# Kernel optimization log

Measured on AMD Instinct MI355X. Metric: run time of the kernel, lower is better.

## Reference

```python
import jax, jax.numpy as jnp
import numpy as np

EPS = 1e-6

def layer_norm(x, g, b):
    m = jnp.mean(x, axis=-1, keepdims=True)
    v = jnp.mean(jnp.square(x - m), axis=-1, keepdims=True)
    return (x - m) * jax.lax.rsqrt(v + EPS) * g + b

def setup_inputs() -> dict:
    key = jax.random.key(0)
    ks = jax.random.split(key, 12)
    B, L, D, Dff, SK = 8, 4096, 512, 2048, 128
    s = 0.02
    return {
        "x": jax.random.normal(ks[0], (B, L, D), jnp.float32),
        "Wq": jax.random.normal(ks[1], (D, D), jnp.float32) * s,
        "bq": jnp.zeros((D,), jnp.float32),
        "Wk": jax.random.normal(ks[2], (D, D), jnp.float32) * s,
        "bk": jnp.zeros((D,), jnp.float32),
        "Wv": jax.random.normal(ks[3], (D, D), jnp.float32) * s,
        "bv": jnp.zeros((D,), jnp.float32),
        "Wo": jax.random.normal(ks[4], (D, D), jnp.float32) * s,
        "bo": jnp.zeros((D,), jnp.float32),
        "g1": jnp.ones((D,), jnp.float32),
        "b1": jnp.zeros((D,), jnp.float32),
        "W1f": jax.random.normal(ks[5], (D, Dff), jnp.float32) * s,
        "b1f": jnp.zeros((Dff,), jnp.float32),
        "W2f": jax.random.normal(ks[6], (Dff, D), jnp.float32) * s,
        "b2f": jnp.zeros((D,), jnp.float32),
        "g2": jnp.ones((D,), jnp.float32),
        "b2": jnp.zeros((D,), jnp.float32),
        "sample_idx": jax.random.randint(ks[7], (SK,), 0, L, jnp.int64),
    }

NUM_HEADS = 8
TOP_U = 128

def prob_sparse_attention(x, Wq, bq, Wk, bk, Wv, bv, Wo, bo, sample_idx):
    B, L, D = x.shape
    H = NUM_HEADS
    dh = D // H
    scale = 1.0 / jnp.sqrt(jnp.asarray(dh, x.dtype))
    # projections -> [B, H, L, dh]
    def split_heads(t):
        return t.reshape(B, L, H, dh).transpose(0, 2, 1, 3)
    Q = split_heads(x @ Wq + bq)
    K = split_heads(x @ Wk + bk)
    V = split_heads(x @ Wv + bv)
    # sparsity measurement on a sampled key subset: [B, H, L, SK]
    K_samp = K[:, :, sample_idx, :]
    s_samp = jnp.einsum('bhld,bhsd->bhls', Q, K_samp)
    M = jnp.max(s_samp, axis=-1) - jnp.mean(s_samp, axis=-1)  # [B, H, L]
    _, top_idx = jax.lax.top_k(M, TOP_U)  # [B, H, u]
    # gather top-u queries: [B, H, u, dh]
    Q_top = jnp.take_along_axis(Q, top_idx[..., None], axis=2)
    scores = jnp.einsum('bhud,bhld->bhul', Q_top, K) * scale  # [B, H, u, L]
    attn = jax.nn.softmax(scores, axis=-1)
    ctx_top = jnp.einsum('bhul,bhld->bhud', attn, V)  # [B, H, u, dh]
    # lazy queries get mean(V)
    meanV = jnp.mean(V, axis=2, keepdims=True)  # [B, H, 1, dh]
    ctx = jnp.broadcast_to(meanV, (B, H, L, dh))
    bi = jnp.arange(B)[:, None, None]
    hi = jnp.arange(H)[None, :, None]
    ctx = ctx.at[bi, hi, top_idx].set(ctx_top)
    out = ctx.transpose(0, 2, 1, 3).reshape(B, L, D)
    return out @ Wo + bo

def reference(x, Wq, bq, Wk, bk, Wv, bv, Wo, bo, g1, b1, W1f, b1f, W2f, b2f, g2, b2, sample_idx):
    attn_out = prob_sparse_attention(x, Wq, bq, Wk, bk, Wv, bv, Wo, bo, sample_idx)
    x1 = layer_norm(x + attn_out, g1, b1)
    ffn = jax.nn.relu(x1 @ W1f + b1f) @ W2f + b2f
    return layer_norm(x1 + ffn, g2, b2)
```

## Files before the change

kernel.cpp:

```cpp
#include <hip/hip_runtime.h>
#include <hip/hip_bf16.h>

using bf16 = __hip_bfloat16;

constexpr int Bd  = 8;
constexpr int Ld  = 4096;
constexpr int Dd  = 512;
constexpr int Hd  = 8;
constexpr int DHd = 64;
constexpr int DFFd= 2048;
constexpr int Ud  = 128;
constexpr int MLd = Bd * Ld;
constexpr int KSd = 16;

typedef short          bf16x8 __attribute__((ext_vector_type(8)));
typedef unsigned short u16x8  __attribute__((ext_vector_type(8)));
typedef float          f32x4  __attribute__((ext_vector_type(4)));

__device__ __forceinline__ float bf2float(bf16 v) { return __bfloat162float(v); }

__device__ __forceinline__ float wred_sum(float v) {
    #pragma unroll
    for (int o = 32; o > 0; o >>= 1) v += __shfl_xor(v, o);
    return v;
}
__device__ __forceinline__ float wred_max(float v) {
    #pragma unroll
    for (int o = 32; o > 0; o >>= 1) v = fmaxf(v, __shfl_xor(v, o));
    return v;
}
__device__ __forceinline__ float scrub(float v) {
    return (fabsf(v) < 1e20f) ? v : 0.0f;
}
__device__ __forceinline__ short f2bs(float f) {
    bf16 h = __float2bfloat16(f);
    return *reinterpret_cast<short*>(&h);
}

__device__ __forceinline__ void gload_lds16(const bf16* g, bf16* lds_base) {
    __builtin_amdgcn_global_load_lds((const __attribute__((address_space(1))) void*)g,
                                     (__attribute__((address_space(3))) void*)lds_base,
                                     16, 0, 0);
}

__global__ void detect_kernel(const void* xraw, int* flags) {
    const unsigned short* u = (const unsigned short*)xraw;
    __shared__ int cnt;
    if (threadIdx.x == 0) cnt = 0;
    __syncthreads();
    int local = 0;
    for (int i = threadIdx.x; i < 1024; i += 256) {
        int e = (u[2 * i] >> 7) & 0xFF;
        if (e >= 96 && e <= 142) local++;
    }
    atomicAdd(&cnt, local);
    __syncthreads();
    if (threadIdx.x == 0) flags[0] = (cnt < 512) ? 1 : 0;
}

__global__ void conv_kernel(const void* raw, bf16* dst, int n, const int* flags) {
    int i = blockIdx.x * 256 + threadIdx.x;
    if (i >= n) return;
    if (flags[0]) dst[i] = __float2bfloat16(((const float*)raw)[i]);
    else          dst[i] = ((const bf16*)raw)[i];
}

__global__ void convT_kernel(const void* raw, bf16* dst, int K, int N, const int* flags) {
    __shared__ bf16 tile[32][33];
    const int k0 = blockIdx.y * 32, n0 = blockIdx.x * 32;
    const int tx = threadIdx.x & 31, ty = threadIdx.x >> 5;
    #pragma unroll
    for (int p = 0; p < 4; ++p) {
        int k = k0 + ty + p * 8, n = n0 + tx;
        float v = flags[0] ? ((const float*)raw)[(size_t)k * N + n]
                           : bf2float(((const bf16*)raw)[(size_t)k * N + n]);
        tile[ty + p * 8][tx] = __float2bfloat16(v);
    }
    __syncthreads();
    #pragma unroll
    for (int p = 0; p < 4; ++p) {
        int n = n0 + ty + p * 8, k = k0 + tx;
        dst[(size_t)n * K + k] = tile[tx][ty + p * 8];
    }
}

__global__ void zero_kernel(int* p, int n) {
    int i = blockIdx.x * 256 + threadIdx.x;
    if (i < n) p[i] = 0;
}

__global__ void idx_kernel(const void* raw, int* out) {
    const int* r32 = (const int*)raw;
    __shared__ int is64;
    int t = threadIdx.x;
    if (t == 0) is64 = 1;
    __syncthreads();
    if (t < 64 && r32[2 * t + 1] != 0) is64 = 0;
    __syncthreads();
    int v = is64 ? r32[2 * t] : r32[t];
    out[t] = min(max(v, 0), Ld - 1);
}

template<bool RELU>
__launch_bounds__(256)
__global__ void mfma_gemm(const bf16* __restrict__ X, const bf16* __restrict__ WT,
                          const bf16* __restrict__ bias, bf16* __restrict__ C,
                          int M, int N, int K)
{
    __shared__ bf16 As[128 * 32];
    __shared__ bf16 Bs[128 * 32];
    const int t = threadIdx.x;
    const int lane = t & 63, wave = t >> 6;
    const int wr = wave >> 1, wc = wave & 1;
    const int quad = lane >> 4, l15 = lane & 15;
    const int m0 = blockIdx.y * 128, n0 = blockIdx.x * 128;
    const int lrow = lane >> 2, lcol = (lane & 3) * 8;

    f32x4 acc[4][4] = {};

    for (int k0 = 0; k0 < K; k0 += 32) {
        #pragma unroll
        for (int p = 0; p < 2; ++p) {
            int r0 = wave * 16 + p * 64;
            gload_lds16(&X [(size_t)(m0 + r0 + lrow) * K + k0 + lcol], &As[r0 * 32]);
            gload_lds16(&WT[(size_t)(n0 + r0 + lrow) * K + k0 + lcol], &Bs[r0 * 32]);
        }
        __syncthreads();
        bf16x8 a[4], b[4];
        #pragma unroll
        for (int i = 0; i < 4; ++i) {
            a[i] = *(const bf16x8*)&As[(wr * 64 + i * 16 + l15) * 32 + quad * 8];
            b[i] = *(const bf16x8*)&Bs[(wc * 64 + i * 16 + l15) * 32 + quad * 8];
        }
        #pragma unroll
        for (int i = 0; i < 4; ++i)
            #pragma unroll
            for (int j = 0; j < 4; ++j)
                acc[i][j] = __builtin_amdgcn_mfma_f32_16x16x32_bf16(a[i], b[j], acc[i][j], 0, 0, 0);
        __syncthreads();
    }
    #pragma unroll
    for (int j = 0; j < 4; ++j) {
        int n = n0 + wc * 64 + j * 16 + l15;
        float bi = bf2float(bias[n]);
        #pragma unroll
        for (int i = 0; i < 4; ++i) {
            #pragma unroll
            for (int r = 0; r < 4; ++r) {
                int m = m0 + wr * 64 + i * 16 + quad * 4 + r;
                float v = acc[i][j][r] + bi;
                if (RELU) v = fmaxf(v, 0.0f);
                C[(size_t)m * N + n] = __float2bfloat16(v);
            }
        }
    }
}

__launch_bounds__(256)
__global__ void m_kernel(const bf16* __restrict__ Q, const bf16* __restrict__ Kg,
                         const int* __restrict__ sidx, float* __restrict__ Mv)
{
    __shared__ float Qs[64][68];
    __shared__ float Ks[64][132];
    __shared__ float redM[64][16];
    __shared__ float redS[64][16];
    const int t  = threadIdx.x;
    const int bh = blockIdx.y, b = bh >> 3, h = bh & 7;
    const int l0 = blockIdx.x * 64;

    int dl = t & 63, r4 = t >> 6;
    #pragma unroll
    for (int p = 0; p < 16; ++p) {
        int lr = r4 + p * 4;
        Qs[dl][lr] = bf2float(Q[((size_t)(b * Ld + l0 + lr)) * Dd + h * 64 + dl]);
    }
    #pragma unroll
    for (int p = 0; p < 32; ++p) {
        int j = r4 + p * 4;
        Ks[dl][j] = bf2float(Kg[((size_t)(b * Ld + sidx[j])) * Dd + h * 64 + dl]);
    }
    __syncthreads();

    const int tx = t & 15, ty = t >> 4;
    float acc[4][8] = {};
    for (int d = 0; d < 64; ++d) {
        float4 a4  = *(const float4*)&Qs[d][ty * 4];
        float4 b4a = *(const float4*)&Ks[d][tx * 8];
        float4 b4b = *(const float4*)&Ks[d][tx * 8 + 4];
        float av[4] = {a4.x, a4.y, a4.z, a4.w};
        float bv[8] = {b4a.x, b4a.y, b4a.z, b4a.w, b4b.x, b4b.y, b4b.z, b4b.w};
        #pragma unroll
        for (int i = 0; i < 4; ++i)
            #pragma unroll
            for (int j = 0; j < 8; ++j)
                acc[i][j] = fmaf(av[i], bv[j], acc[i][j]);
    }
    #pragma unroll
    for (int i = 0; i < 4; ++i) {
        float rmax = -1e30f, rsum = 0.0f;
        #pragma unroll
        for (int j = 0; j < 8; ++j) { rmax = fmaxf(rmax, acc[i][j]); rsum += acc[i][j]; }
        redM[ty * 4 + i][tx] = rmax;
        redS[ty * 4 + i][tx] = rsum;
    }
    __syncthreads();
    if (t < 64) {
        float m = -1e30f, s = 0.0f;
        #pragma unroll
        for (int q = 0; q < 16; ++q) { m = fmaxf(m, redM[t][q]); s += redS[t][q]; }
        Mv[(size_t)bh * Ld + l0 + t] = m - s * (1.0f / 128.0f);
    }
}

__launch_bounds__(256)
__global__ void topk_kernel(const float* __restrict__ Mv, int* __restrict__ topIdx)
{
    __shared__ unsigned ukey[4096];
    __shared__ short listA[4096], listB[4096];
    __shared__ int hist[256];
    __shared__ int outCnt, candCnt, selB, aboveK;
    const int bh = blockIdx.x, t = threadIdx.x;

    for (int i = t; i < 4096; i += 256) {
        unsigned u = __float_as_uint(Mv[(size_t)bh * Ld + i]);
        ukey[i] = (u & 0x80000000u) ? ~u : (u | 0x80000000u);
    }
    if (t == 0) outCnt = 0;
    __syncthreads();

    int K = Ud;
    #pragma unroll
    for (int r = 0; r < 4; ++r) {
        const int shift = 24 - 8 * r;
        hist[t] = 0;
        __syncthreads();
        const int n = (r == 0) ? 4096 : candCnt;
        const short* cur = (r & 1) ? listB : listA;
        for (int i = t; i < n; i += 256) {
            int idx = (r == 0) ? i : cur[i];
            atomicAdd(&hist[(ukey[idx] >> shift) & 0xFF], 1);
        }
        __syncthreads();
        if (t == 0) {
            int cum = 0, b = 255;
            for (; b > 0; --b) {
                if (cum + hist[b] >= K) break;
                cum += hist[b];
            }
            selB = b; aboveK = cum; candCnt = 0;
        }
        __syncthreads();
        const int sb = selB;
        short* nxt = (r & 1) ? listA : listB;
        for (int i = t; i < n; i += 256) {
            int idx = (r == 0) ? i : cur[i];
            int by = (ukey[idx] >> shift) & 0xFF;
            if (by > sb) {
                int p = atomicAdd(&outCnt, 1);
                topIdx[bh * Ud + p] = idx;
            } else if (by == sb) {
                int p = atomicAdd(&candCnt, 1);
                nxt[p] = (short)idx;
            }
        }
        __syncthreads();
        K -= aboveK;
        if (K == 0) break;
    }
    if (K > 0) {
        for (int i = t; i < K; i += 256) {
            int p = atomicAdd(&outCnt, 1);
            topIdx[bh * Ud + p] = listA[i];
        }
    }
}

__global__ void rows_kernel(const int* __restrict__ topIdx, int* __restrict__ rowCnt,
                            int* __restrict__ rowEnt)
{
    const int bh = blockIdx.x, u = threadIdx.x, b = bh >> 3;
    const int lq = topIdx[bh * Ud + u];
    const int row = b * Ld + lq;
    int slot = atomicAdd(&rowCnt[row], 1) & 7;
    rowEnt[row * 8 + slot] = bh * Ud + u;
}

__launch_bounds__(256)
__global__ void meanv_kernel(const bf16* __restrict__ V, float* __restrict__ meanV)
{
    const int bh = blockIdx.x, b = bh >> 3, h = bh & 7;
    const int l0 = blockIdx.y * 64;
    const int t = threadIdx.x;
    const int d = t & 63, part = t >> 6;
    float s = 0.0f;
    #pragma unroll
    for (int p = 0; p < 16; ++p) {
        int l = l0 + part + p * 4;
        s += bf2float(V[((size_t)(b * Ld + l)) * Dd + h * 64 + d]);
    }
    __shared__ float red[256];
    red[t] = s;
    __syncthreads();
    if (t < 64) {
        float tot = red[t] + red[64 + t] + red[128 + t] + red[192 + t];
        atomicAdd(&meanV[bh * 64 + t], tot * (1.0f / 4096.0f));
    }
}

__launch_bounds__(256, 3)
__global__ void attn_kernel(const bf16* __restrict__ Qg, const bf16* __restrict__ Kg,
                            const bf16* __restrict__ Vg, const int* __restrict__ topIdx,
                            bf16* __restrict__ pO, float* __restrict__ pM, float* __restrict__ pL)
{
    __shared__ __align__(16) short KsS[2][64 * 64];
    __shared__ __align__(16) short VsS[2][64 * 72];
    __shared__ __align__(16) short PsS[4][32 * 72];

    const int t = threadIdx.x, lane = t & 63, w = t >> 6;
    const int l15 = lane & 15, quad = lane >> 4;
    const int bh = blockIdx.x, ks = blockIdx.y;
    const int b = bh >> 3, h = bh & 7;
    const int key0 = ks * (Ld / KSd);
    constexpr int NT = (Ld / KSd) / 64;

    bf16x8 qf[2][2];
    #pragma unroll
    for (int m = 0; m < 2; ++m) {
        const int u  = w * 32 + m * 16 + l15;
        const int lq = topIdx[bh * Ud + u];
        const bf16* qr = Qg + ((size_t)(b * Ld + lq)) * Dd + h * 64;
        qf[m][0] = *(const bf16x8*)(qr + quad * 8);
        qf[m][1] = *(const bf16x8*)(qr + 32 + quad * 8);
    }

    const int vkey = t >> 2, vd0 = (t & 3) * 16;
    u16x8 vr0, vr1;

    auto loadV = [&](int tt) {
        const bf16* vs = Vg + ((size_t)(b * Ld + key0 + tt * 64 + vkey)) * Dd + h * 64 + vd0;
        vr0 = *(const u16x8*)vs;
        vr1 = *(const u16x8*)(vs + 8);
    };
    auto stageK = [&](int buf, int tt) {
        const int kb0 = key0 + tt * 64;
        #pragma unroll
        for (int sz = 0; sz < 2; ++sz) {
            const int sg = w * 2 + sz;
            const int r  = sg * 8 + (lane >> 3);
            const int cs = (lane & 7) ^ (lane >> 3);
            gload_lds16(Kg + ((size_t)(b * Ld + kb0 + r)) * Dd + h * 64 + cs * 8,
                        (bf16*)&KsS[buf][sg * 512]);
        }
    };
    auto writeV = [&](int buf) {
        #pragma unroll
        for (int j = 0; j < 8; ++j) {
            VsS[buf][(vd0 + j) * 72 + vkey]     = (short)vr0[j];
            VsS[buf][(vd0 + 8 + j) * 72 + vkey] = (short)vr1[j];
        }
    };

    float mrun[2][4], lrun[2][4];
    f32x4 o[2][4] = {};
    #pragma unroll
    for (int m = 0; m < 2; ++m)
        #pragma unroll
        for (int r = 0; r < 4; ++r) { mrun[m][r] = -1e30f; lrun[m][r] = 0.0f; }

    loadV(0); stageK(0, 0); writeV(0);
    __syncthreads();

    short* PsW = &PsS[w][0];
    for (int tt = 0; tt < NT; ++tt) {
        const int cur = tt & 1;
        if (tt + 1 < NT) { loadV(tt + 1); stageK(cur ^ 1, tt + 1); }

        const short* KsB = &KsS[cur][0];
        f32x4 s[2][4] = {};
        #pragma unroll
        for (int kk = 0; kk < 2; ++kk) {
            bf16x8 kb[4];
            #pragma unroll
            for (int n = 0; n < 4; ++n)
                kb[n] = *(const bf16x8*)&KsB[(n * 16 + l15) * 64 +
                                             (((kk * 4 + quad) ^ (l15 & 7)) * 8)];
            #pragma unroll
            for (int m = 0; m < 2; ++m)
                #pragma unroll
                for (int n = 0; n < 4; ++n)
                    s[m][n] = __builtin_amdgcn_mfma_f32_16x16x32_bf16(qf[m][kk], kb[n], s[m][n], 0, 0, 0);
        }

        #pragma unroll
        for (int m = 0; m < 2; ++m) {
            #pragma unroll
            for (int r = 0; r < 4; ++r) {
                float sv[4];
                #pragma unroll
                for (int n = 0; n < 4; ++n) sv[n] = s[m][n][r] * 0.125f;
                float vm = fmaxf(fmaxf(sv[0], sv[1]), fmaxf(sv[2], sv[3]));
                #pragma unroll
                for (int off = 1; off < 16; off <<= 1) vm = fmaxf(vm, __shfl_xor(vm, off));
                const float mn = fmaxf(mrun[m][r], vm);
                const float al = __expf(mrun[m][r] - mn);
                float ps = 0.0f;
                #pragma unroll
                for (int n = 0; n < 4; ++n) { sv[n] = __expf(sv[n] - mn); ps += sv[n]; }
                #pragma unroll
                for (int off = 1; off < 16; off <<= 1) ps += __shfl_xor(ps, off);
                lrun[m][r] = lrun[m][r] * al + ps;
                mrun[m][r] = mn;
                const int qrow = m * 16 + quad * 4 + r;
                #pragma unroll
                for (int n = 0; n < 4; ++n) {
                    PsW[qrow * 72 + n * 16 + l15] = f2bs(sv[n]);
                    o[m][n][r] *= al;
                }
            }
        }

        if (tt + 1 < NT) writeV(cur ^ 1);

        const short* VsB = &VsS[cur][0];
        #pragma unroll
        for (int kk = 0; kk < 2; ++kk) {
            bf16x8 pa[2], vb[4];
            #pragma unroll
            for (int m = 0; m < 2; ++m)
                pa[m] = *(const bf16x8*)&PsW[(m * 16 + l15) * 72 + kk * 32 + quad * 8];
            #pragma unroll
            for (int n = 0; n < 4; ++n)
                vb[n] = *(const bf16x8*)&VsB[(n * 16 + l15) * 72 + kk * 32 + quad * 8];
            #pragma unroll
            for (int m = 0; m < 2; ++m)
                #pragma unroll
                for (int n = 0; n < 4; ++n)
                    o[m][n] = __builtin_amdgcn_mfma_f32_16x16x32_bf16(pa[m], vb[n], o[m][n], 0, 0, 0);
        }
        __syncthreads();
    }

    const size_t pbase = ((size_t)(ks * 64 + bh)) * Ud;
    #pragma unroll
    for (int m = 0; m < 2; ++m) {
        #pragma unroll
        for (int r = 0; r < 4; ++r) {
            const int u = w * 32 + m * 16 + quad * 4 + r;
            #pragma unroll
            for (int n = 0; n < 4; ++n)
                pO[(pbase + u) * 64 + n * 16 + l15] = __float2bfloat16(o[m][n][r]);
            if (l15 == 0) { pM[pbase + u] = mrun[m][r]; pL[pbase + u] = lrun[m][r]; }
        }
    }
}

__global__ void combine_kernel(const bf16* __restrict__ pO, const float* __restrict__ pM,
                               const float* __restrict__ pL, float* __restrict__ ctxTop)
{
    const int u = blockIdx.x & 127, bh = blockIdx.x >> 7, c = threadIdx.x;
    float mstar = -1e30f;
    #pragma unroll
    for (int ks = 0; ks < KSd; ++ks)
        mstar = fmaxf(mstar, pM[(ks * 64 + bh) * Ud + u]);
    float lsum = 0.0f, osum = 0.0f;
    #pragma unroll
    for (int ks = 0; ks < KSd; ++ks) {
        float wgt = __expf(pM[(ks * 64 + bh) * Ud + u] - mstar);
        lsum += pL[(ks * 64 + bh) * Ud + u] * wgt;
        osum += bf2float(pO[(((size_t)ks * 64 + bh) * Ud + u) * 64 + c]) * wgt;
    }
    ctxTop[((size_t)bh * Ud + u) * 64 + c] = scrub(osum / lsum);
}

__launch_bounds__(512)
__global__ void baseout_kernel(const float* __restrict__ meanV, const bf16* __restrict__ Wo,
                               const bf16* __restrict__ bo, float* __restrict__ baseOut)
{
    const int b = blockIdx.x, t = threadIdx.x;
    __shared__ float mv[512];
    mv[t] = meanV[b * 512 + t];
    __syncthreads();
    float acc = bf2float(bo[t]);
    for (int d = 0; d < 512; ++d)
        acc = fmaf(mv[d], bf2float(Wo[(size_t)d * 512 + t]), acc);
    baseOut[b * 512 + t] = acc;
}

__launch_bounds__(256)
__global__ void delta_kernel(const float* __restrict__ ctxTop, const float* __restrict__ meanV,
                             const bf16* __restrict__ Wo, bf16* __restrict__ deltaOut)
{
    const int u = blockIdx.x, bh = blockIdx.y, h = bh & 7, t = threadIdx.x;
    __shared__ float diff[64];
    if (t < 64) diff[t] = ctxTop[((size_t)bh * Ud + u) * 64 + t] - meanV[bh * 64 + t];
    __syncthreads();
    for (int n = t; n < 512; n += 256) {
        float acc = 0.0f;
        #pragma unroll 8
        for (int dd = 0; dd < 64; ++dd)
            acc = fmaf(diff[dd], bf2float(Wo[(size_t)(h * 64 + dd) * 512 + n]), acc);
        deltaOut[((size_t)bh * Ud + u) * 512 + n] = __float2bfloat16(acc);
    }
}

__launch_bounds__(256)
__global__ void ln1_kernel(const bf16* __restrict__ x, const float* __restrict__ baseOut,
                           const int* __restrict__ rowCnt, const int* __restrict__ rowEnt,
                           const bf16* __restrict__ deltaOut,
                           const bf16* __restrict__ g, const bf16* __restrict__ bb,
                           bf16* __restrict__ x1)
{
    const int row = blockIdx.x, t = threadIdx.x;
    const int b = row >> 12;
    const size_t base = (size_t)row * 512;
    float v0 = bf2float(x[base + t])       + baseOut[b * 512 + t];
    float v1 = bf2float(x[base + t + 256]) + baseOut[b * 512 + t + 256];
    const int cnt = min(rowCnt[row], 8);
    for (int e = 0; e < cnt; ++e) {
        const bf16* dr = &deltaOut[(size_t)rowEnt[row * 8 + e] * 512];
        v0 += bf2float(dr[t]);
        v1 += bf2float(dr[t + 256]);
    }
    v0 = scrub(v0); v1 = scrub(v1);
    float s = v0 + v1, q = v0 * v0 + v1 * v1;
    s = wred_sum(s); q = wred_sum(q);
    __shared__ float sred[4], qred[4];
    int lane = t & 63, w = t >> 6;
    if (lane == 0) { sred[w] = s; qred[w] = q; }
    __syncthreads();
    float tot  = sred[0] + sred[1] + sred[2] + sred[3];
    float totq = qred[0] + qred[1] + qred[2] + qred[3];
    float mean = tot * (1.0f / 512.0f);
    float var  = fmaxf(totq * (1.0f / 512.0f) - mean * mean, 0.0f);
    float rstd = rsqrtf(var + 1e-6f);
    x1[base + t]       = __float2bfloat16((v0 - mean) * rstd * bf2float(g[t])       + bf2float(bb[t]));
    x1[base + t + 256] = __float2bfloat16((v1 - mean) * rstd * bf2float(g[t + 256]) + bf2float(bb[t + 256]));
}

__launch_bounds__(256)
__global__ void ln2_kernel(const bf16* __restrict__ x1, const bf16* __restrict__ ffn,
                           const bf16* __restrict__ g, const bf16* __restrict__ bb,
                           void* __restrict__ out, const int* __restrict__ flags)
{
    const int row = blockIdx.x, t = threadIdx.x;
    const size_t base = (size_t)row * 512;
    float v0 = bf2float(x1[base + t])       + bf2float(ffn[base + t]);
    float v1 = bf2float(x1[base + t + 256]) + bf2float(ffn[base + t + 256]);
    v0 = scrub(v0); v1 = scrub(v1);
    float s = v0 + v1, q = v0 * v0 + v1 * v1;
    s = wred_sum(s); q = wred_sum(q);
    __shared__ float sred[4], qred[4];
    int lane = t & 63, w = t >> 6;
    if (lane == 0) { sred[w] = s; qred[w] = q; }
    __syncthreads();
    float tot  = sred[0] + sred[1] + sred[2] + sred[3];
    float totq = qred[0] + qred[1] + qred[2] + qred[3];
    float mean = tot * (1.0f / 512.0f);
    float var  = fmaxf(totq * (1.0f / 512.0f) - mean * mean, 0.0f);
    float rstd = rsqrtf(var + 1e-6f);
    float o0 = (v0 - mean) * rstd * bf2float(g[t])       + bf2float(bb[t]);
    float o1 = (v1 - mean) * rstd * bf2float(g[t + 256]) + bf2float(bb[t + 256]);
    if (flags[0]) {
        ((float*)out)[base + t]       = o0;
        ((float*)out)[base + t + 256] = o1;
    } else {
        ((bf16*)out)[base + t]       = __float2bfloat16(o0);
        ((bf16*)out)[base + t + 256] = __float2bfloat16(o1);
    }
}

extern "C" void kernel_launch(void* const* d_in, const int* in_sizes, int n_in,
                              void* d_out, int out_size, void* d_ws, size_t ws_size,
                              hipStream_t stream)
{
    const void* sraw = d_in[17];

    const size_t NQ = (size_t)MLd * Dd;
    char* w = (char*)d_ws;
    size_t off = 0;
    auto alloc = [&](size_t bytes) { void* p = w + off; off += (bytes + 63) & ~size_t(63); return p; };
    bf16*  Qb   = (bf16*)alloc(NQ * 2);
    bf16*  Kb   = (bf16*)alloc(NQ * 2);
    bf16*  Vb   = (bf16*)alloc(NQ * 2);
    bf16*  xc   = (bf16*)alloc(NQ * 2);
    bf16*  WTq  = (bf16*)alloc(Dd * Dd * 2);
    bf16*  WTk  = (bf16*)alloc(Dd * Dd * 2);
    bf16*  WTv  = (bf16*)alloc(Dd * Dd * 2);
    bf16*  Woc  = (bf16*)alloc(Dd * Dd * 2);
    bf16*  WT1f = (bf16*)alloc((size_t)Dd * DFFd * 2);
    bf16*  WT2f = (bf16*)alloc((size_t)DFFd * Dd * 2);
    bf16* bqc = (bf16*)alloc(Dd * 2);
    bf16* bkc = (bf16*)alloc(Dd * 2);
    bf16* bvc = (bf16*)alloc(Dd * 2);
    bf16* boc = (bf16*)alloc(Dd * 2);
    bf16* g1c = (bf16*)alloc(Dd * 2);
    bf16* b1c = (bf16*)alloc(Dd * 2);
    bf16* b1fc= (bf16*)alloc(DFFd * 2);
    bf16* b2fc= (bf16*)alloc(Dd * 2);
    bf16* g2c = (bf16*)alloc(Dd * 2);
    bf16* b2c = (bf16*)alloc(Dd * 2);
    bf16*  pOb     = (bf16*)alloc((size_t)KSd * 64 * Ud * 64 * 2);
    float* Mv      = (float*)alloc((size_t)Bd * Hd * Ld * 4);
    float* ctxTop  = (float*)alloc((size_t)Bd * Hd * Ud * DHd * 4);
    float* meanV   = (float*)alloc(Bd * Hd * DHd * 4);
    float* baseOut = (float*)alloc(Bd * Dd * 4);
    int*   topIdx  = (int*)alloc(Bd * Hd * Ud * 4);
    int*   sidx    = (int*)alloc(128 * 4);
    int*   rowCnt  = (int*)alloc(MLd * 4);
    int*   rowEnt  = (int*)alloc(MLd * 8 * 4);
    int*   flags   = (int*)alloc(64);
    bf16*  x1b  = Vb;
    bf16*  h1b  = Qb;
    bf16*  ffnb = xc;
    bf16*  deltaOut = pOb;
    float* pM = Mv;
    float* pL = Mv + KSd * 64 * Ud;

    if (off > ws_size) return;

    detect_kernel<<<1, 256, 0, stream>>>(d_in[0], flags);

    auto conv = [&](int i, bf16* dst, int n) {
        conv_kernel<<<(n + 255) / 256, 256, 0, stream>>>(d_in[i], dst, n, flags);
    };
    conv(0,  xc, (int)NQ);
    convT_kernel<<<dim3(Dd / 32, Dd / 32), 256, 0, stream>>>(d_in[1], WTq, Dd, Dd, flags);
    convT_kernel<<<dim3(Dd / 32, Dd / 32), 256, 0, stream>>>(d_in[3], WTk, Dd, Dd, flags);
    convT_kernel<<<dim3(Dd / 32, Dd / 32), 256, 0, stream>>>(d_in[5], WTv, Dd, Dd, flags);
    convT_kernel<<<dim3(DFFd / 32, Dd / 32), 256, 0, stream>>>(d_in[11], WT1f, Dd, DFFd, flags);
    convT_kernel<<<dim3(Dd / 32, DFFd / 32), 256, 0, stream>>>(d_in[13], WT2f, DFFd, Dd, flags);
    conv(7,  Woc, Dd * Dd);
    conv(2,  bqc, Dd);  conv(4,  bkc, Dd);  conv(6,  bvc, Dd);  conv(8,  boc, Dd);
    conv(9,  g1c, Dd);  conv(10, b1c, Dd);
    conv(12, b1fc, DFFd); conv(14, b2fc, Dd);
    conv(15, g2c, Dd);  conv(16, b2c, Dd);

    zero_kernel<<<(MLd + 255) / 256, 256, 0, stream>>>(rowCnt, MLd);
    zero_kernel<<<(Bd * Hd * DHd + 255) / 256, 256, 0, stream>>>((int*)meanV, Bd * Hd * DHd);
    idx_kernel<<<1, 128, 0, stream>>>(sraw, sidx);

    mfma_gemm<false><<<dim3(4, 256), 256, 0, stream>>>(xc, WTq, bqc, Qb, MLd, Dd, Dd);
    mfma_gemm<false><<<dim3(4, 256), 256, 0, stream>>>(xc, WTk, bkc, Kb, MLd, Dd, Dd);
    mfma_gemm<false><<<dim3(4, 256), 256, 0, stream>>>(xc, WTv, bvc, Vb, MLd, Dd, Dd);

    m_kernel<<<dim3(Ld / 64, Bd * Hd), 256, 0, stream>>>(Qb, Kb, sidx, Mv);
    topk_kernel<<<Bd * Hd, 256, 0, stream>>>(Mv, topIdx);
    rows_kernel<<<Bd * Hd, 128, 0, stream>>>(topIdx, rowCnt, rowEnt);
    meanv_kernel<<<dim3(Bd * Hd, Ld / 64), 256, 0, stream>>>(Vb, meanV);

    attn_kernel<<<dim3(Bd * Hd, KSd), 256, 0, stream>>>(Qb, Kb, Vb, topIdx, pOb, pM, pL);
    combine_kernel<<<Bd * Hd * Ud, 64, 0, stream>>>(pOb, pM, pL, ctxTop);

    baseout_kernel<<<Bd, 512, 0, stream>>>(meanV, Woc, boc, baseOut);
    delta_kernel<<<dim3(Ud, Bd * Hd), 256, 0, stream>>>(ctxTop, meanV, Woc, deltaOut);

    ln1_kernel<<<MLd, 256, 0, stream>>>(xc, baseOut, rowCnt, rowEnt, deltaOut, g1c, b1c, x1b);

    for (int c = 0; c < 2; ++c) {
        mfma_gemm<true ><<<dim3(16, 128), 256, 0, stream>>>(
            x1b + (size_t)c * 16384 * 512, WT1f, b1fc, h1b, 16384, DFFd, Dd);
        mfma_gemm<false><<<dim3(4, 128), 256, 0, stream>>>(
            h1b, WT2f, b2fc, ffnb + (size_t)c * 16384 * 512, 16384, Dd, DFFd);
    }

    ln2_kernel<<<MLd, 256, 0, stream>>>(x1b, ffnb, g2c, b2c, d_out, flags);
}
```

Before: 813.6 us.

## Compute sampled Q·K sparsity scores with bf16 MFMA and swizzled LDS tiles

Rewrites the sparsity-measurement kernel so the Q × sampled-K product runs on MFMA bf16 instructions instead of scalar fp32 FMAs. Tiles are loaded directly into LDS as bf16 with an XOR swizzle, and each block now handles 128 query rows. Row max and mean are reduced with cross-lane shuffles instead of a shared-memory reduction. This targets the FMA-bound inner loop and the LDS traffic of fp32 staging. The trade-off is bf16 inputs to the score products, which are already stored as bf16, so accuracy should be similar; near-tie ordering for top-k could still differ slightly.

```diff
diff --git a/kernel.cpp b/kernel.cpp
--- a/kernel.cpp
+++ b/kernel.cpp
@@ -160,55 +160,69 @@
 __global__ void m_kernel(const bf16* __restrict__ Q, const bf16* __restrict__ Kg,
                          const int* __restrict__ sidx, float* __restrict__ Mv)
 {
-    __shared__ float Qs[64][68];
-    __shared__ float Ks[64][132];
-    __shared__ float redM[64][16];
-    __shared__ float redS[64][16];
-    const int t  = threadIdx.x;
+    __shared__ __align__(16) short Qs[128 * 64];
+    __shared__ __align__(16) short Ks[128 * 64];
+    __shared__ int sidxs[128];
+
+    const int t = threadIdx.x, lane = t & 63, w = t >> 6;
+    const int l15 = lane & 15, quad = lane >> 4;
+    const int l0 = blockIdx.x * 128;
     const int bh = blockIdx.y, b = bh >> 3, h = bh & 7;
-    const int l0 = blockIdx.x * 64;
-
-    int dl = t & 63, r4 = t >> 6;
-    #pragma unroll
-    for (int p = 0; p < 16; ++p) {
-        int lr = r4 + p * 4;
-        Qs[dl][lr] = bf2float(Q[((size_t)(b * Ld + l0 + lr)) * Dd + h * 64 + dl]);
-    }
-    #pragma unroll
-    for (int p = 0; p < 32; ++p) {
-        int j = r4 + p * 4;
-        Ks[dl][j] = bf2float(Kg[((size_t)(b * Ld + sidx[j])) * Dd + h * 64 + dl]);
-    }
-    __syncthreads();
-
-    const int tx = t & 15, ty = t >> 4;
-    float acc[4][8] = {};
-    for (int d = 0; d < 64; ++d) {
-        float4 a4  = *(const float4*)&Qs[d][ty * 4];
-        float4 b4a = *(const float4*)&Ks[d][tx * 8];
-        float4 b4b = *(const float4*)&Ks[d][tx * 8 + 4];
-        float av[4] = {a4.x, a4.y, a4.z, a4.w};
-        float bv[8] = {b4a.x, b4a.y, b4a.z, b4a.w, b4b.x, b4b.y, b4b.z, b4b.w};
-        #pragma unroll
-        for (int i = 0; i < 4; ++i)
-            #pragma unroll
-            for (int j = 0; j < 8; ++j)
-                acc[i][j] = fmaf(av[i], bv[j], acc[i][j]);
-    }
-    #pragma unroll
-    for (int i = 0; i < 4; ++i) {
-        float rmax = -1e30f, rsum = 0.0f;
-        #pragma unroll
-        for (int j = 0; j < 8; ++j) { rmax = fmaxf(rmax, acc[i][j]); rsum += acc[i][j]; }
-        redM[ty * 4 + i][tx] = rmax;
-        redS[ty * 4 + i][tx] = rsum;
-    }
-    __syncthreads();
-    if (t < 64) {
-        float m = -1e30f, s = 0.0f;
-        #pragma unroll
-        for (int q = 0; q < 16; ++q) { m = fmaxf(m, redM[t][q]); s += redS[t][q]; }
-        Mv[(size_t)bh * Ld + l0 + t] = m - s * (1.0f / 128.0f);
+
+    if (t < 128) sidxs[t] = sidx[t];
+    __syncthreads();
+
+    const int rseg = lane >> 3;
+    const int cs   = (lane & 7) ^ rseg;
+    #pragma unroll
+    for (int sg4 = 0; sg4 < 4; ++sg4) {
+        const int sg = w * 4 + sg4;
+        const int r  = sg * 8 + rseg;
+        gload_lds16(Q  + ((size_t)(b * Ld + l0 + r))    * Dd + h * 64 + cs * 8,
+                    (bf16*)&Qs[sg * 512]);
+        gload_lds16(Kg + ((size_t)(b * Ld + sidxs[r])) * Dd + h * 64 + cs * 8,
+                    (bf16*)&Ks[sg * 512]);
+    }
+    __syncthreads();
+
+    f32x4 s[2][8] = {};
+    #pragma unroll
+    for (int kk = 0; kk < 2; ++kk) {
+        const int ch = ((kk * 4 + quad) ^ (l15 & 7)) * 8;
+        bf16x8 qa[2], kb[8];
+        #pragma unroll
+        for (int mt = 0; mt < 2; ++mt)
+            qa[mt] = *(const bf16x8*)&Qs[(w * 32 + mt * 16 + l15) * 64 + ch];
+        #pragma unroll
+        for (int nt = 0; nt < 8; ++nt)
+            kb[nt] = *(const bf16x8*)&Ks[(nt * 16 + l15) * 64 + ch];
+        #pragma unroll
+        for (int mt = 0; mt < 2; ++mt)
+            #pragma unroll
+            for (int nt = 0; nt < 8; ++nt)
+                s[mt][nt] = __builtin_amdgcn_mfma_f32_16x16x32_bf16(qa[mt], kb[nt], s[mt][nt], 0, 0, 0);
+    }
+
+    #pragma unroll
+    for (int mt = 0; mt < 2; ++mt) {
+        #pragma unroll
+        for (int r = 0; r < 4; ++r) {
+            float vmax = -1e30f, vsum = 0.0f;
+            #pragma unroll
+            for (int nt = 0; nt < 8; ++nt) {
+                float v = s[mt][nt][r];
+                vmax = fmaxf(vmax, v); vsum += v;
+            }
+            #pragma unroll
+            for (int off = 1; off < 16; off <<= 1) {
+                vmax = fmaxf(vmax, __shfl_xor(vmax, off));
+                vsum += __shfl_xor(vsum, off);
+            }
+            if (l15 == 0) {
+                const int row = w * 32 + mt * 16 + quad * 4 + r;
+                Mv[(size_t)bh * Ld + l0 + row] = vmax - vsum * (1.0f / 128.0f);
+            }
+        }
     }
 }
 
@@ -643,7 +657,7 @@
     mfma_gemm<false><<<dim3(4, 256), 256, 0, stream>>>(xc, WTk, bkc, Kb, MLd, Dd, Dd);
     mfma_gemm<false><<<dim3(4, 256), 256, 0, stream>>>(xc, WTv, bvc, Vb, MLd, Dd, Dd);
 
-    m_kernel<<<dim3(Ld / 64, Bd * Hd), 256, 0, stream>>>(Qb, Kb, sidx, Mv);
+    m_kernel<<<dim3(Ld / 128, Bd * Hd), 256, 0, stream>>>(Qb, Kb, sidx, Mv);
     topk_kernel<<<Bd * Hd, 256, 0, stream>>>(Mv, topIdx);
     rows_kernel<<<Bd * Hd, 128, 0, stream>>>(topIdx, rowCnt, rowEnt);
     meanv_kernel<<<dim3(Bd * Hd, Ld / 64), 256, 0, stream>>>(Vb, meanV);
```

Measured after the change: 763.0 us. 6.2% less time.
